# Kernel optimization log

Hardware: AMD Instinct MI355X
Metric: run time of the kernel (lower is better)

## Reference

```python
import jax, jax.numpy as jnp
import numpy as np

B, N, C, H = 8, 1024, 768, 12
WBITS, ABITS, PGABITS = 8, 8, 4
TH = 0.99  # greater-than mask threshold on MSB softmax


def quant(x, bits):
    """Fixed-point quantize to `bits` bits, straight-through estimator."""
    step = 2.0 ** (1 - bits)
    q = jnp.round(x / step) * step
    return x + jax.lax.stop_gradient(q - x)


def setup_inputs() -> dict:
    key = jax.random.key(0)
    k1, k2, k3 = jax.random.split(key, 3)
    x = jax.random.normal(k1, (B, N, C), jnp.float32)
    # qkv: QLinear(dim, 3*dim, bias=False); proj: QLinear(dim, dim, bias=True)
    w_qkv = jax.random.normal(k2, (3 * C, C), jnp.float32) * (C ** -0.5)
    w_proj = jax.random.normal(k3, (C, C), jnp.float32) * (C ** -0.5)
    b_proj = jnp.zeros((C,), jnp.float32)
    return {"x": x, "w_qkv": w_qkv, "w_proj": w_proj, "b_proj": b_proj}


def reference(x, w_qkv, w_proj, b_proj):
    d = C // H
    scale = d ** -0.5
    # QLinear: quantize activations and weights, then matmul (no qkv bias)
    qkv = quant(x, ABITS) @ quant(w_qkv, WBITS).T            # [B,N,3C]
    qkv = qkv.reshape(B, N, 3, H, d).transpose(2, 0, 3, 1, 4)  # [3,B,H,N,d]
    qkv = quant(qkv, ABITS)
    q, k, v = qkv[0], qkv[1], qkv[2]
    # low-precision MSB pass
    q_msb = quant(q, PGABITS)
    k_msb = quant(k, PGABITS)
    attn_msb = jax.nn.softmax(
        jnp.einsum('bhqd,bhkd->bhqk', q_msb, k_msb) * scale, axis=-1)
    # GreaterThan with straight-through backward (identity grad)
    gt = (attn_msb > TH).astype(attn_msb.dtype)
    mask = attn_msb + jax.lax.stop_gradient(gt - attn_msb)
    # full-precision pass, masked pre-softmax
    attn = jnp.einsum('bhqd,bhkd->bhqk', q, k) * scale * mask
    attn = quant(jax.nn.softmax(attn, axis=-1), ABITS)
    out = jnp.einsum('bhqk,bhkd->bhqd', attn, v)             # [B,H,N,d]
    out = out.transpose(0, 2, 1, 3).reshape(B, N, C)
    return quant(out, ABITS) @ quant(w_proj, WBITS).T + b_proj
```

## Files before the change

### kernel.cpp

```cpp
#include <hip/hip_runtime.h>

#define NB 8
#define NSEQ 1024
#define NC 768
#define NH 12
#define ND 64
#define NM 8192

typedef _Float16 v8h __attribute__((ext_vector_type(8)));
typedef float v4f __attribute__((ext_vector_type(4)));
typedef int   v4i __attribute__((ext_vector_type(4)));

__device__ __forceinline__ float q8f(float x){ return rintf(x*128.f)*0.0078125f; }
__device__ __forceinline__ int imax2(int a, int b){ return a > b ? a : b; }
__device__ __forceinline__ int imin2(int a, int b){ return a < b ? a : b; }

__device__ __forceinline__ int swz(int r, int g){ return (r<<6) + (((g ^ (r & 7)) & 7)<<3); }

__device__ __forceinline__ void async_cp16(const void* g, void* l) {
  __builtin_amdgcn_global_load_lds(
      (const __attribute__((address_space(1))) unsigned int*)g,
      (__attribute__((address_space(3))) unsigned int*)l, 16, 0, 0);
}

__device__ __forceinline__ int idot64(const int* a, const int* b) {
  int si = 0;
#if __has_builtin(__builtin_amdgcn_sdot4)
#pragma unroll
  for (int j = 0; j < 16; j++) si = __builtin_amdgcn_sdot4(a[j], b[j], si, false);
#else
  const char* ca = (const char*)a;
  const char* cb = (const char*)b;
#pragma unroll
  for (int j = 0; j < 64; j++) si += (int)ca[j] * (int)cb[j];
#endif
  return si;
}

__global__ __launch_bounds__(256) void k_pre(const float* __restrict__ x,
                                             const float* __restrict__ wq,
                                             const float* __restrict__ bias,
                                             _Float16* __restrict__ xt,
                                             _Float16* __restrict__ wqt,
                                             float* __restrict__ out) {
  int b = blockIdx.x;
  if (b < 3648) {
    const float* src; _Float16* dst; int gid;
    if (b < 3072) { src = x;  dst = xt;  gid = b*256 + threadIdx.x; }
    else          { src = wq; dst = wqt; gid = (b-3072)*256 + threadIdx.x; }
    int tile = gid / 12288;
    int rem  = gid - tile*12288;
    int chunk = rem >> 10, idx = rem & 1023;
    int r = idx >> 3, g = idx & 7;
    const float* s = src + (size_t)(tile*128 + r)*768 + chunk*64 + g*8;
    float4 v0 = *(const float4*)s, v1 = *(const float4*)(s + 4);
    v8h o;
    o[0]=(_Float16)q8f(v0.x); o[1]=(_Float16)q8f(v0.y); o[2]=(_Float16)q8f(v0.z); o[3]=(_Float16)q8f(v0.w);
    o[4]=(_Float16)q8f(v1.x); o[5]=(_Float16)q8f(v1.y); o[6]=(_Float16)q8f(v1.z); o[7]=(_Float16)q8f(v1.w);
    *(v8h*)&dst[((size_t)tile*12 + chunk)*8192 + swz(r, g)] = o;
  } else {
    int gid = (b - 3648)*256 + threadIdx.x;
    int c4 = gid % 192;
    ((float4*)out)[gid] = ((const float4*)bias)[c4];
  }
}

__device__ __forceinline__ void mfma_tile(const _Float16* Ah, const _Float16* Bh,
                                          int WR0, int l15, int quad, v4f acc[2][8]) {
#pragma unroll
  for (int ks = 0; ks < 2; ks++) {
    v8h a0 = *(const v8h*)&Ah[swz(WR0 + l15,      ks*4 + quad)];
    v8h a1 = *(const v8h*)&Ah[swz(WR0 + 16 + l15, ks*4 + quad)];
#pragma unroll
    for (int nt = 0; nt < 8; nt++) {
      v8h b = *(const v8h*)&Bh[swz(nt*16 + l15, ks*4 + quad)];
      acc[0][nt] = __builtin_amdgcn_mfma_f32_16x16x32_f16(a0, b, acc[0][nt], 0, 0, 0);
      acc[1][nt] = __builtin_amdgcn_mfma_f32_16x16x32_f16(a1, b, acc[1][nt], 0, 0, 0);
    }
  }
}

__global__ __launch_bounds__(256) void k_qk(const _Float16* __restrict__ xt,
                                            const _Float16* __restrict__ wqt,
                                            char* __restrict__ QmI,
                                            char* __restrict__ KmI) {
  __shared__ _Float16 S[2][16384];
  const int tid  = threadIdx.x;
  const int lane = tid & 63;
  const int quad = lane >> 4;
  const int l15  = lane & 15;
  const int wid  = tid >> 6;
  const int WR0  = wid * 32;
  const int m0 = blockIdx.x * 128, n0 = blockIdx.y * 128;
  const _Float16* Asrc = xt  + (size_t)blockIdx.x * 12 * 8192;
  const _Float16* Bsrc = wqt + (size_t)blockIdx.y * 12 * 8192;

  auto stage = [&](int kc, int bi) {
    const _Float16* a = Asrc + kc*8192;
    const _Float16* bsc = Bsrc + kc*8192;
#pragma unroll
    for (int s = 0; s < 8; s++) {
      int seg = wid*8 + s;
      const _Float16* g = (seg < 16 ? a + seg*512 : bsc + (seg-16)*512) + lane*8;
      async_cp16(g, &S[bi][seg*512]);
    }
  };

  v4f acc[2][8] = {};
  stage(0, 0);
#pragma unroll 1
  for (int kc = 0; kc < 12; kc++) {
    if (kc + 1 < 12) {
      stage(kc + 1, (kc + 1) & 1);
      asm volatile("s_waitcnt vmcnt(8)" ::: "memory");
    } else {
      asm volatile("s_waitcnt vmcnt(0)" ::: "memory");
    }
    __builtin_amdgcn_s_barrier();
    mfma_tile(&S[kc & 1][0], &S[kc & 1][8192], WR0, l15, quad, acc);
    __builtin_amdgcn_s_barrier();
  }

  const int which = (n0 >= 768);
  char* P8 = (char*)&S[0][0];
  __syncthreads();
#pragma unroll
  for (int mt = 0; mt < 2; mt++)
#pragma unroll
    for (int nt = 0; nt < 8; nt++)
#pragma unroll
      for (int rr = 0; rr < 4; rr++) {
        float v = q8f(acc[mt][nt][rr]);
        int qi = (int)rintf(v * 8.f);
        P8[(WR0 + mt*16 + quad*4 + rr)*144 + nt*16 + l15] = (char)qi;
      }
  __syncthreads();
  int c0 = n0 - which*768;
#pragma unroll
  for (int t = 0; t < 4; t++) {
    int idx = tid + t*256;
    int r = idx >> 3, cg = idx & 7;
    v4i val = *(const v4i*)&P8[r*144 + cg*16];
    if (which == 0) {
      *(v4i*)&QmI[(size_t)(m0 + r)*768 + c0 + cg*16] = val;
    } else {
      int m = m0 + r, n = m & 1023, bI = m >> 10;
      int h = (c0 + cg*16) >> 6, d0 = (cg & 3)*16;
      *(v4i*)&KmI[(((size_t)(bI*NH + h)*1024 + n) << 6) + d0] = val;
    }
  }
}

__global__ __launch_bounds__(256) void k_attn(const char* __restrict__ QmI,
                                              const char* __restrict__ KmI,
                                              const float* __restrict__ x,
                                              const float* __restrict__ wqkv,
                                              const float* __restrict__ wproj,
                                              float* __restrict__ out) {
  __shared__ char  S2[2][16384];
  __shared__ float rowm[128];
  __shared__ int   cand[128];
  __shared__ int   hrowA[128];
  __shared__ int   hcolA[128];
  __shared__ float qf[64], kf[64], vf[64];
  __shared__ float od[64];
  __shared__ float pps;
  __shared__ int   cnt, hcnt;

  const int tid  = threadIdx.x;
  const int lane = tid & 63;
  const int quad = lane >> 4;
  const int l15  = lane & 15;
  const int wid  = tid >> 6;
  const int R0   = wid * 16;
  const int bh = blockIdx.x;
  const int q0 = blockIdx.y * 128;
  const int bb = bh / NH, hb = bh % NH;
  const size_t mrow = (size_t)bb * NSEQ;
  const int hoff = hb * 64;
  const char* KmB = KmI + (size_t)bh * 1024 * 64;

  if (tid == 0) { cnt = 0; hcnt = 0; }

  auto stageK = [&](int kp, int bi) {
#pragma unroll
    for (int s = 0; s < 4; s++) {
      int seg = wid*4 + s;
      async_cp16(KmB + kp*16384 + seg*1024 + lane*16, &S2[bi][seg*1024]);
    }
  };

  v4i aQ[2];
#pragma unroll
  for (int b2 = 0; b2 < 2; b2++)
    aQ[b2] = *(const v4i*)&QmI[(mrow + q0 + b2*64 + R0 + l15)*768 + hoff + quad*16];

  int lm[2][4], lm2[2][4];
#pragma unroll
  for (int b2 = 0; b2 < 2; b2++)
#pragma unroll
    for (int r = 0; r < 4; r++) { lm[b2][r] = -1073741824; lm2[b2][r] = -1073741824; }

  stageK(0, 0);
#pragma unroll 1
  for (int kp = 0; kp < 4; kp++) {
    if (kp + 1 < 4) {
      stageK(kp + 1, (kp + 1) & 1);
      asm volatile("s_waitcnt vmcnt(4)" ::: "memory");
    } else {
      asm volatile("s_waitcnt vmcnt(0)" ::: "memory");
    }
    __builtin_amdgcn_s_barrier();
#pragma unroll
    for (int g64 = 0; g64 < 4; g64++) {
      const char* Ks = &S2[kp & 1][g64*4096];
      v4i c0a[4] = {}, c1a[4] = {};
      __builtin_amdgcn_s_setprio(1);
#pragma unroll
      for (int nt = 0; nt < 4; nt++) {
        v4i b = *(const v4i*)&Ks[(nt*16 + l15)*64 + quad*16];
        c0a[nt] = __builtin_amdgcn_mfma_i32_16x16x64_i8(aQ[0], b, c0a[nt], 0, 0, 0);
        c1a[nt] = __builtin_amdgcn_mfma_i32_16x16x64_i8(aQ[1], b, c1a[nt], 0, 0, 0);
      }
      __builtin_amdgcn_s_setprio(0);
#pragma unroll
      for (int r = 0; r < 4; r++) {
        int g0 = imax2(imax2(c0a[0][r], c0a[1][r]), imax2(c0a[2][r], c0a[3][r]));
        lm2[0][r] = imax2(lm2[0][r], imin2(lm[0][r], g0));
        lm[0][r]  = imax2(lm[0][r], g0);
        int g1 = imax2(imax2(c1a[0][r], c1a[1][r]), imax2(c1a[2][r], c1a[3][r]));
        lm2[1][r] = imax2(lm2[1][r], imin2(lm[1][r], g1));
        lm[1][r]  = imax2(lm[1][r], g1);
      }
    }
    __builtin_amdgcn_s_barrier();
  }
#pragma unroll
  for (int b2 = 0; b2 < 2; b2++)
#pragma unroll
    for (int r = 0; r < 4; r++) {
      int m = lm[b2][r], m2 = lm2[b2][r];
#pragma unroll
      for (int o = 1; o < 16; o <<= 1) {
        int om  = __shfl_xor(m, o);
        int om2 = __shfl_xor(m2, o);
        m2 = imax2(imax2(m2, om2), imin2(m, om));
        m  = imax2(m, om);
      }
      if (l15 == 0 && (m - m2) > 2304) {
        int row = b2*64 + R0 + quad*4 + r;
        rowm[row] = (float)m * 0.001953125f;
        int ix = atomicAdd(&cnt, 1);
        cand[ix] = row;
      }
    }
  __syncthreads();

  int nc = cnt;
  for (int ci = wid; ci < nc; ci += 4) {
    int row = cand[ci];
    float m = rowm[row];
    const int* qrow = (const int*)&QmI[(mrow + q0 + row)*768 + hoff];
    int qw[16];
#pragma unroll
    for (int j = 0; j < 16; j++) qw[j] = qrow[j];
    float l = 0.f, bmax = -1e30f;
    int bcol = 0;
    for (int t = 0; t < 16; t++) {
      const int* kb = (const int*)&KmB[(size_t)(t*64 + lane)*64];
      int si = idot64(qw, kb);
      float s = (float)si * 0.001953125f;
      l += expf(s - m);
      if (s > bmax) { bmax = s; bcol = t*64 + lane; }
    }
#pragma unroll
    for (int o = 1; o < 64; o <<= 1) {
      l += __shfl_xor(l, o);
      float ov = __shfl_xor(bmax, o);
      int   oc = __shfl_xor(bcol, o);
      if (ov > bmax || (ov == bmax && oc < bcol)) { bmax = ov; bcol = oc; }
    }
    if (lane == 0 && (1.0f / l) > 0.99f) {
      int ix = atomicAdd(&hcnt, 1);
      hrowA[ix] = row; hcolA[ix] = bcol;
    }
  }
  __syncthreads();

  int nh = hcnt;
  for (int hi = 0; hi < nh; hi++) {
    int row = hrowA[hi], cst = hcolA[hi];
    if (tid < 192) {
      int d = tid & 63, part = tid >> 6;
      int wrow = part*768 + hoff + d;
      int xrow = (part == 0) ? (int)(mrow + q0 + row) : (int)(mrow + cst);
      const float* xr = &x[(size_t)xrow*768];
      const float* wr = &wqkv[(size_t)wrow*768];
      float s = 0.f;
      for (int k = 0; k < 768; k++) s += q8f(xr[k]) * q8f(wr[k]);
      float v = q8f(s);
      if (part == 0) qf[d] = v; else if (part == 1) kf[d] = v; else vf[d] = v;
    }
    __syncthreads();
    if (tid == 0) {
      float s = 0.f;
      for (int d = 0; d < 64; d++) s += qf[d]*kf[d];
      float sf = s * 0.125f;
      float m2 = fmaxf(sf, 0.f);
      float l2 = expf(sf - m2) + 1023.f*expf(-m2);
      pps = rintf(expf(sf - m2)/l2*128.f)*0.0078125f;
    }
    __syncthreads();
    float p = pps;
    if (p != 0.f) {
      if (tid < 64) od[tid] = q8f(p * vf[tid]);
      __syncthreads();
      for (int c = tid; c < 768; c += 256) {
        const float* wr = &wproj[(size_t)c*768 + hoff];
        float s = 0.f;
        for (int d = 0; d < 64; d++) s += od[d] * q8f(wr[d]);
        atomicAdd(&out[(mrow + q0 + row)*768 + c], s);
      }
    }
    __syncthreads();
  }
}

extern "C" void kernel_launch(void* const* d_in, const int* in_sizes, int n_in,
                              void* d_out, int out_size, void* d_ws, size_t ws_size,
                              hipStream_t stream) {
  const float* x      = (const float*)d_in[0];
  const float* w_qkv  = (const float*)d_in[1];
  const float* w_proj = (const float*)d_in[2];
  const float* b_proj = (const float*)d_in[3];
  float* out = (float*)d_out;

  char* p = (char*)d_ws;
  _Float16* xt  = (_Float16*)p;  p += (size_t)NM*768*2;
  _Float16* wqt = (_Float16*)p;  p += (size_t)1536*768*2;
  char* QmI = p;  p += (size_t)NM*768;
  char* KmI = p;  p += (size_t)NM*768;

  dim3 blk(256);
  k_pre <<<dim3(9792), blk, 0, stream>>>(x, w_qkv, b_proj, xt, wqt, out);
  k_qk  <<<dim3(64, 12), blk, 0, stream>>>(xt, wqt, QmI, KmI);
  k_attn<<<dim3(96, 8), blk, 0, stream>>>(QmI, KmI, x, w_qkv, w_proj, out);
}
```

Before: 122.6 us.

## Enlarge QK projection GEMM to 256x256 tiles with 8 waves and fold bias init

The QK projection GEMM moves from 128x128 tiles with 4 waves to 256x256 tiles with 8 waves (512 threads). B fragments are held in registers, and the A and B async loads for the next k-chunk are split across the compute phase, with setprio around the MFMA bursts. The output bias fill moves from k_pre into extra blocks of k_qk, so k_pre only converts x and w_qkv. The goal is more data reuse per LDS load. The trade-off is that the GEMM now has only 192 tiles and 128KB of LDS per block, which may leave many CUs idle and limit occupancy.

```diff
diff --git a/kernel.cpp b/kernel.cpp
--- a/kernel.cpp
+++ b/kernel.cpp
@@ -39,113 +39,143 @@
 
 __global__ __launch_bounds__(256) void k_pre(const float* __restrict__ x,
                                              const float* __restrict__ wq,
-                                             const float* __restrict__ bias,
                                              _Float16* __restrict__ xt,
-                                             _Float16* __restrict__ wqt,
-                                             float* __restrict__ out) {
+                                             _Float16* __restrict__ wqt) {
   int b = blockIdx.x;
-  if (b < 3648) {
-    const float* src; _Float16* dst; int gid;
-    if (b < 3072) { src = x;  dst = xt;  gid = b*256 + threadIdx.x; }
-    else          { src = wq; dst = wqt; gid = (b-3072)*256 + threadIdx.x; }
-    int tile = gid / 12288;
-    int rem  = gid - tile*12288;
-    int chunk = rem >> 10, idx = rem & 1023;
-    int r = idx >> 3, g = idx & 7;
-    const float* s = src + (size_t)(tile*128 + r)*768 + chunk*64 + g*8;
-    float4 v0 = *(const float4*)s, v1 = *(const float4*)(s + 4);
-    v8h o;
-    o[0]=(_Float16)q8f(v0.x); o[1]=(_Float16)q8f(v0.y); o[2]=(_Float16)q8f(v0.z); o[3]=(_Float16)q8f(v0.w);
-    o[4]=(_Float16)q8f(v1.x); o[5]=(_Float16)q8f(v1.y); o[6]=(_Float16)q8f(v1.z); o[7]=(_Float16)q8f(v1.w);
-    *(v8h*)&dst[((size_t)tile*12 + chunk)*8192 + swz(r, g)] = o;
-  } else {
-    int gid = (b - 3648)*256 + threadIdx.x;
+  const float* src; _Float16* dst; int gid;
+  if (b < 3072) { src = x;  dst = xt;  gid = b*256 + threadIdx.x; }
+  else          { src = wq; dst = wqt; gid = (b-3072)*256 + threadIdx.x; }
+  int tile = gid / 12288;
+  int rem  = gid - tile*12288;
+  int chunk = rem >> 10, idx = rem & 1023;
+  int r = idx >> 3, g = idx & 7;
+  const float* s = src + (size_t)(tile*128 + r)*768 + chunk*64 + g*8;
+  float4 v0 = *(const float4*)s, v1 = *(const float4*)(s + 4);
+  v8h o;
+  o[0]=(_Float16)q8f(v0.x); o[1]=(_Float16)q8f(v0.y); o[2]=(_Float16)q8f(v0.z); o[3]=(_Float16)q8f(v0.w);
+  o[4]=(_Float16)q8f(v1.x); o[5]=(_Float16)q8f(v1.y); o[6]=(_Float16)q8f(v1.z); o[7]=(_Float16)q8f(v1.w);
+  *(v8h*)&dst[((size_t)tile*12 + chunk)*8192 + swz(r, g)] = o;
+}
+
+__global__ __launch_bounds__(512, 2) void k_qk(const _Float16* __restrict__ xt,
+                                               const _Float16* __restrict__ wqt,
+                                               const float* __restrict__ bias,
+                                               char* __restrict__ QmI,
+                                               char* __restrict__ KmI,
+                                               float* __restrict__ out) {
+  if (blockIdx.x >= 192) {
+    int gid = (blockIdx.x - 192)*512 + threadIdx.x;
     int c4 = gid % 192;
     ((float4*)out)[gid] = ((const float4*)bias)[c4];
-  }
-}
-
-__device__ __forceinline__ void mfma_tile(const _Float16* Ah, const _Float16* Bh,
-                                          int WR0, int l15, int quad, v4f acc[2][8]) {
-#pragma unroll
-  for (int ks = 0; ks < 2; ks++) {
-    v8h a0 = *(const v8h*)&Ah[swz(WR0 + l15,      ks*4 + quad)];
-    v8h a1 = *(const v8h*)&Ah[swz(WR0 + 16 + l15, ks*4 + quad)];
-#pragma unroll
-    for (int nt = 0; nt < 8; nt++) {
-      v8h b = *(const v8h*)&Bh[swz(nt*16 + l15, ks*4 + quad)];
-      acc[0][nt] = __builtin_amdgcn_mfma_f32_16x16x32_f16(a0, b, acc[0][nt], 0, 0, 0);
-      acc[1][nt] = __builtin_amdgcn_mfma_f32_16x16x32_f16(a1, b, acc[1][nt], 0, 0, 0);
-    }
-  }
-}
-
-__global__ __launch_bounds__(256) void k_qk(const _Float16* __restrict__ xt,
-                                            const _Float16* __restrict__ wqt,
-                                            char* __restrict__ QmI,
-                                            char* __restrict__ KmI) {
-  __shared__ _Float16 S[2][16384];
+    return;
+  }
+  __shared__ _Float16 S[65536];
+  _Float16* SA = S;
+  _Float16* SB = S + 32768;
+
   const int tid  = threadIdx.x;
   const int lane = tid & 63;
   const int quad = lane >> 4;
   const int l15  = lane & 15;
   const int wid  = tid >> 6;
-  const int WR0  = wid * 32;
-  const int m0 = blockIdx.x * 128, n0 = blockIdx.y * 128;
-  const _Float16* Asrc = xt  + (size_t)blockIdx.x * 12 * 8192;
-  const _Float16* Bsrc = wqt + (size_t)blockIdx.y * 12 * 8192;
-
-  auto stage = [&](int kc, int bi) {
-    const _Float16* a = Asrc + kc*8192;
-    const _Float16* bsc = Bsrc + kc*8192;
-#pragma unroll
-    for (int s = 0; s < 8; s++) {
-      int seg = wid*8 + s;
-      const _Float16* g = (seg < 16 ? a + seg*512 : bsc + (seg-16)*512) + lane*8;
-      async_cp16(g, &S[bi][seg*512]);
+  const int wm   = wid >> 2;
+  const int wn   = wid & 3;
+  const int bx = blockIdx.x & 31, by = blockIdx.x >> 5;
+  const int m0 = bx * 256, n0 = by * 256;
+
+  const _Float16* Abase = xt  + (size_t)(2*bx) * 12 * 8192;
+  const _Float16* Bbase = wqt + (size_t)(2*by) * 12 * 8192;
+
+  auto stage_half = [&](const _Float16* src, _Float16* dst) {
+#pragma unroll
+    for (int s = 0; s < 2; s++) {
+      int base = (wid*2 + s)*512;
+      async_cp16(src + base + lane*8, dst + base);
     }
   };
 
-  v4f acc[2][8] = {};
-  stage(0, 0);
+  v4f acc[8][4] = {};
+
+  stage_half(Abase,               SA);
+  stage_half(Abase + 12*8192,     SA + 8192);
+  stage_half(Bbase,               SB);
+  stage_half(Bbase + 12*8192,     SB + 8192);
+  asm volatile("s_waitcnt vmcnt(0)" ::: "memory");
+  __builtin_amdgcn_s_barrier();
+
 #pragma unroll 1
   for (int kc = 0; kc < 12; kc++) {
+    const int buf = kc & 1;
+    const _Float16* A  = &SA[(buf*2 + wm)*8192];
+    const _Float16* Bh = &SB[(buf*2 + (wn>>1))*8192];
+    _Float16* SAn = &SA[(buf^1)*16384];
+    _Float16* SBn = &SB[(buf^1)*16384];
+
     if (kc + 1 < 12) {
-      stage(kc + 1, (kc + 1) & 1);
-      asm volatile("s_waitcnt vmcnt(8)" ::: "memory");
-    } else {
-      asm volatile("s_waitcnt vmcnt(0)" ::: "memory");
-    }
+      stage_half(Abase + (size_t)(kc+1)*8192,        SAn);
+      stage_half(Abase + (size_t)(12 + kc+1)*8192,   SAn + 8192);
+    }
+
+    v8h bf[4][2];
+#pragma unroll
+    for (int nt = 0; nt < 4; nt++)
+#pragma unroll
+      for (int ks = 0; ks < 2; ks++)
+        bf[nt][ks] = *(const v8h*)&Bh[swz((wn&1)*64 + nt*16 + l15, ks*4 + quad)];
+
+#pragma unroll
+    for (int p = 0; p < 4; p++) {
+      v8h a[2][2];
+#pragma unroll
+      for (int mt = 0; mt < 2; mt++)
+#pragma unroll
+        for (int ks = 0; ks < 2; ks++)
+          a[mt][ks] = *(const v8h*)&A[swz((p*2 + mt)*16 + l15, ks*4 + quad)];
+      __builtin_amdgcn_s_setprio(1);
+#pragma unroll
+      for (int ks = 0; ks < 2; ks++)
+#pragma unroll
+        for (int nt = 0; nt < 4; nt++) {
+          acc[p*2+0][nt] = __builtin_amdgcn_mfma_f32_16x16x32_f16(a[0][ks], bf[nt][ks], acc[p*2+0][nt], 0, 0, 0);
+          acc[p*2+1][nt] = __builtin_amdgcn_mfma_f32_16x16x32_f16(a[1][ks], bf[nt][ks], acc[p*2+1][nt], 0, 0, 0);
+        }
+      __builtin_amdgcn_s_setprio(0);
+      if (p == 0 && kc + 1 < 12) {
+        stage_half(Bbase + (size_t)(kc+1)*8192,        SBn);
+        stage_half(Bbase + (size_t)(12 + kc+1)*8192,   SBn + 8192);
+      }
+    }
+    asm volatile("s_waitcnt vmcnt(0)" ::: "memory");
     __builtin_amdgcn_s_barrier();
-    mfma_tile(&S[kc & 1][0], &S[kc & 1][8192], WR0, l15, quad, acc);
-    __builtin_amdgcn_s_barrier();
-  }
-
-  const int which = (n0 >= 768);
-  char* P8 = (char*)&S[0][0];
+  }
+
+  char* P8 = (char*)S;
+#pragma unroll
+  for (int fr = 0; fr < 8; fr++)
+#pragma unroll
+    for (int nt = 0; nt < 4; nt++)
+#pragma unroll
+      for (int rr = 0; rr < 4; rr++) {
+        float v = q8f(acc[fr][nt][rr]);
+        int qi = (int)rintf(v * 8.f);
+        int rl = wm*128 + fr*16 + quad*4 + rr;
+        int cl = wn*64 + nt*16 + l15;
+        P8[rl*272 + cl] = (char)qi;
+      }
   __syncthreads();
-#pragma unroll
-  for (int mt = 0; mt < 2; mt++)
-#pragma unroll
-    for (int nt = 0; nt < 8; nt++)
-#pragma unroll
-      for (int rr = 0; rr < 4; rr++) {
-        float v = q8f(acc[mt][nt][rr]);
-        int qi = (int)rintf(v * 8.f);
-        P8[(WR0 + mt*16 + quad*4 + rr)*144 + nt*16 + l15] = (char)qi;
-      }
-  __syncthreads();
+  const int which = (by >= 3);
   int c0 = n0 - which*768;
 #pragma unroll
-  for (int t = 0; t < 4; t++) {
-    int idx = tid + t*256;
-    int r = idx >> 3, cg = idx & 7;
-    v4i val = *(const v4i*)&P8[r*144 + cg*16];
-    if (which == 0) {
+  for (int t = 0; t < 8; t++) {
+    int idx = tid + t*512;
+    int r = idx >> 4, cg = idx & 15;
+    v4i val = *(const v4i*)&P8[r*272 + cg*16];
+    if (!which) {
       *(v4i*)&QmI[(size_t)(m0 + r)*768 + c0 + cg*16] = val;
     } else {
       int m = m0 + r, n = m & 1023, bI = m >> 10;
-      int h = (c0 + cg*16) >> 6, d0 = (cg & 3)*16;
+      int col = c0 + cg*16;
+      int h = col >> 6, d0 = col & 63;
       *(v4i*)&KmI[(((size_t)(bI*NH + h)*1024 + n) << 6) + d0] = val;
     }
   }
@@ -341,8 +371,7 @@
   char* QmI = p;  p += (size_t)NM*768;
   char* KmI = p;  p += (size_t)NM*768;
 
-  dim3 blk(256);
-  k_pre <<<dim3(9792), blk, 0, stream>>>(x, w_qkv, b_proj, xt, wqt, out);
-  k_qk  <<<dim3(64, 12), blk, 0, stream>>>(xt, wqt, QmI, KmI);
-  k_attn<<<dim3(96, 8), blk, 0, stream>>>(QmI, KmI, x, w_qkv, w_proj, out);
-}
+  k_pre <<<dim3(3648), dim3(256), 0, stream>>>(x, w_qkv, xt, wqt);
+  k_qk  <<<dim3(192 + 3072), dim3(512), 0, stream>>>(xt, wqt, b_proj, QmI, KmI, out);
+  k_attn<<<dim3(96, 8), dim3(256), 0, stream>>>(QmI, KmI, x, w_qkv, w_proj, out);
+}
```

New measurement: 121.4 us. No clear change (-1.0%).
